# Kernel tuning notes

Measured on AMD Instinct MI355X. Metric: run time of the kernel, lower is better.

## Reference

```python
import jax, jax.numpy as jnp
import numpy as np

B, Q, K, H = 4, 128, 1024, 256
QS, KS, DV = 256, 256, 256


def setup_inputs() -> dict:
    key = jax.random.key(0)
    k1, k2, k3, k4, k5, k6, k7 = jax.random.split(key, 7)
    return {
        "queries": jax.random.normal(k1, (B, Q, QS), dtype=jnp.float32),
        "keys": jax.random.normal(k2, (B, K, KS), dtype=jnp.float32),
        "values": jax.random.normal(k3, (B, K, DV), dtype=jnp.float32),
        "valid_lens": jax.random.randint(k4, (B,), 1, K, dtype=jnp.int64),
        "Wq": jax.random.normal(k5, (QS, H), dtype=jnp.float32) / np.sqrt(QS),
        "Wk": jax.random.normal(k6, (KS, H), dtype=jnp.float32) / np.sqrt(KS),
        "Wv": jax.random.normal(k7, (H,), dtype=jnp.float32) / np.sqrt(H),
    }


def reference(queries, keys, values, valid_lens, Wq, Wk, Wv):
    # Projections: [B,Q,H] and [B,K,H]
    q = jnp.einsum("bqe,eh->bqh", queries, Wq)
    k = jnp.einsum("bke,eh->bkh", keys, Wk)
    # Broadcast add + tanh: [B,Q,K,H] intermediate (the kernel-headroom op)
    feats = jnp.tanh(q[:, :, None, :] + k[:, None, :, :])
    # hidden -> 1 reduction: scores [B,Q,K]
    scores = jnp.einsum("bqkh,h->bqk", feats, Wv)
    # masked softmax: positions >= valid_len set to -1e6 (as in sequence_mask)
    mask = jnp.arange(scores.shape[-1])[None, None, :] < valid_lens[:, None, None]
    scores = jnp.where(mask, scores, jnp.float32(-1e6))
    attn = jax.nn.softmax(scores, axis=-1)
    # dropout is identity in eval mode
    return jnp.einsum("bqk,bkv->bqv", attn, values)
```

## Files before the change

### kernel.cpp

```cpp
#include <hip/hip_runtime.h>

#define NB 4
#define NQ 128
#define NK 1024
#define NH 256
#define NE 256
#define NV 256

#define TSCALE 2.8853900817779268f
#define LOG2E  1.4426950408889634f

static __device__ __forceinline__ float fexp2(float x){ return __builtin_amdgcn_exp2f(x); }
static __device__ __forceinline__ float frcp (float x){ return __builtin_amdgcn_rcpf(x); }
static __device__ __forceinline__ float expT(float x){ return fexp2(x * TSCALE); }

__global__ __launch_bounds__(256) void proj_kernel(
    const float* __restrict__ qin, const float* __restrict__ kin,
    const float* __restrict__ Wq, const float* __restrict__ Wk,
    const float* __restrict__ Wv,
    float4* __restrict__ qEa, float4* __restrict__ kEt) {
    const int tid = threadIdx.x;
    const int bi  = blockIdx.x;
    __shared__ float tr[NH][9];
    if (bi < NB * 32) {
        const int row0 = bi * 4;
        const float* r0 = qin + row0 * NE;
        float a0 = 0.f, a1 = 0.f, a2 = 0.f, a3 = 0.f;
#pragma unroll 2
        for (int e = 0; e < NE; e += 4) {
            float4 q0 = *(const float4*)(r0 + e);
            float4 q1 = *(const float4*)(r0 + NE + e);
            float4 q2 = *(const float4*)(r0 + 2 * NE + e);
            float4 q3 = *(const float4*)(r0 + 3 * NE + e);
#pragma unroll
            for (int j = 0; j < 4; ++j) {
                float w = Wq[(e + j) * NH + tid];
                a0 = fmaf(((const float*)&q0)[j], w, a0);
                a1 = fmaf(((const float*)&q1)[j], w, a1);
                a2 = fmaf(((const float*)&q2)[j], w, a2);
                a3 = fmaf(((const float*)&q3)[j], w, a3);
            }
        }
        qEa[bi * NH + tid] = make_float4(expT(a0), expT(a1),
                                         expT(a2), expT(a3));
    } else {
        const int kb = bi - NB * 32;
        const int b  = kb >> 7;
        const int k0 = (kb & 127) * 8;
        const int c   = k0 >> 6;
        const int kl0 = k0 & 63;
        const float* kr = kin + (b * NK + k0) * NE;
        float acc[8] = {0.f,0.f,0.f,0.f,0.f,0.f,0.f,0.f};
#pragma unroll 2
        for (int e = 0; e < NE; e += 4) {
            float4 kvv[8];
#pragma unroll
            for (int i = 0; i < 8; ++i) kvv[i] = *(const float4*)(kr + i * NE + e);
#pragma unroll
            for (int j = 0; j < 4; ++j) {
                float w = Wk[(e + j) * NH + tid];
#pragma unroll
                for (int i = 0; i < 8; ++i)
                    acc[i] = fmaf(((const float*)&kvv[i])[j], w, acc[i]);
            }
        }
#pragma unroll
        for (int i = 0; i < 8; ++i) tr[tid][i] = expT(acc[i]);
        __syncthreads();
#pragma unroll
        for (int p = 0; p < 2; ++p) {
            int idx2 = p * 256 + tid;
            int hg = idx2 >> 3;
            int kk = idx2 & 7;
            float4 v = make_float4(tr[hg*4+0][kk], tr[hg*4+1][kk],
                                   tr[hg*4+2][kk], tr[hg*4+3][kk]);
            kEt[((b * 16 + c) * 64 + hg) * 64 + kl0 + kk] = v;
        }
    }
}

__global__ __launch_bounds__(256) void attn_kernel(
    const float4* __restrict__ qEa,
    const float4* __restrict__ kEt, const float* __restrict__ V,
    const int* __restrict__ vlen, const float4* __restrict__ Wv4,
    float* __restrict__ part_m, float* __restrict__ part_s,
    float* __restrict__ part_pv) {
    const int tid = threadIdx.x, lane = tid & 63, wvid = tid >> 6;
    const int n0 = (vlen[0] + 63) >> 6, n1 = (vlen[1] + 63) >> 6;
    const int n2 = (vlen[2] + 63) >> 6, n3 = (vlen[3] + 63) >> 6;
    const int G  = n0 + n1 + n2 + n3;
    const int bi = blockIdx.x;
    const int xcd = bi & 7;
    const int jj  = bi >> 3;
    const int qq  = jj & 31;
    const int gs  = ((jj >> 5) << 3) + xcd;
    if (gs >= G) return;
    int b, chunk;
    if      (gs < n0)           { b = 0; chunk = gs; }
    else if (gs < n0 + n1)      { b = 1; chunk = gs - n0; }
    else if (gs < n0 + n1 + n2) { b = 2; chunk = gs - n0 - n1; }
    else                        { b = 3; chunk = gs - n0 - n1 - n2; }
    const int vl    = vlen[b];
    const int k0    = chunk * 64;
    const int k     = k0 + lane;
    const int pidx  = (b * 32 + qq) * 16 + chunk;
    float* pm  = part_m + pidx * 4;
    float* ps  = part_s + pidx * 4;
    float* ppv = part_pv + pidx * (4 * NV);

    __shared__ float red17[4][64 * 17];
    __shared__ float pwT[64][4];
    __shared__ float4 qL[NH];

    qL[tid] = qEa[(b * 32 + qq) * NH + tid];
    __syncthreads();

    const float4* kp = kEt + ((b * 16 + chunk) * 64 + wvid * 16) * 64 + lane;
    float acc0 = 0.f, acc1 = 0.f, acc2 = 0.f, acc3 = 0.f;
#pragma unroll
    for (int i = 0; i < 16; ++i) {
        float4 kv4 = kp[i * 64];
        const int h4 = wvid * 16 + i;
        float4 wv4 = Wv4[h4];
#pragma unroll
        for (int j = 0; j < 4; ++j) {
            float kv  = (j==0)?kv4.x:(j==1)?kv4.y:(j==2)?kv4.z:kv4.w;
            float wvj = (j==0)?wv4.x:(j==1)?wv4.y:(j==2)?wv4.z:wv4.w;
            float4 qa = qL[h4 * 4 + j];
            float t0 = fmaf(qa.x, kv, 1.0f);
            float t1 = fmaf(qa.y, kv, 1.0f);
            float t2 = fmaf(qa.z, kv, 1.0f);
            float t3 = fmaf(qa.w, kv, 1.0f);
            float ab = t0 * t1, cd = t2 * t3;
            float rw = wvj * frcp(ab * cd);
            float rab = rw * cd, rcd = rw * ab;
            acc0 = fmaf(rab, t1, acc0);
            acc1 = fmaf(rab, t0, acc1);
            acc2 = fmaf(rcd, t3, acc2);
            acc3 = fmaf(rcd, t2, acc3);
        }
    }
    {
        float* hp = &red17[wvid][lane * 17];
        hp[0] = acc0; hp[1] = acc1; hp[2] = acc2; hp[3] = acc3;
    }
    __syncthreads();
    {
        const int row = wvid;
        float s = red17[0][lane * 17 + row] + red17[1][lane * 17 + row]
                + red17[2][lane * 17 + row] + red17[3][lane * 17 + row];
        s = (k < vl) ? (-2.0f * s) : -1e30f;
        float m = s;
#pragma unroll
        for (int d = 32; d >= 1; d >>= 1) m = fmaxf(m, __shfl_xor(m, d, 64));
        float p = fexp2((s - m) * LOG2E);
        float u = p;
#pragma unroll
        for (int d = 32; d >= 1; d >>= 1) u += __shfl_xor(u, d, 64);
        if (lane == 0) { pm[row] = m; ps[row] = u; }
        pwT[lane][row] = p;
    }
    __syncthreads();
    {
        const float* Vb = V + (b * NK + k0) * NV;
        const int v4 = lane * 4;
        float4 o0 = {0,0,0,0}, o1 = {0,0,0,0}, o2 = {0,0,0,0}, o3 = {0,0,0,0};
#pragma unroll 4
        for (int kk = 0; kk < 16; ++kk) {
            const int kkk = wvid * 16 + kk;
            float4 pv = *(const float4*)&pwT[kkk][0];
            float4 vv = *(const float4*)&Vb[kkk * NV + v4];
            o0.x = fmaf(pv.x, vv.x, o0.x); o0.y = fmaf(pv.x, vv.y, o0.y);
            o0.z = fmaf(pv.x, vv.z, o0.z); o0.w = fmaf(pv.x, vv.w, o0.w);
            o1.x = fmaf(pv.y, vv.x, o1.x); o1.y = fmaf(pv.y, vv.y, o1.y);
            o1.z = fmaf(pv.y, vv.z, o1.z); o1.w = fmaf(pv.y, vv.w, o1.w);
            o2.x = fmaf(pv.z, vv.x, o2.x); o2.y = fmaf(pv.z, vv.y, o2.y);
            o2.z = fmaf(pv.z, vv.z, o2.z); o2.w = fmaf(pv.z, vv.w, o2.w);
            o3.x = fmaf(pv.w, vv.x, o3.x); o3.y = fmaf(pv.w, vv.y, o3.y);
            o3.z = fmaf(pv.w, vv.z, o3.z); o3.w = fmaf(pv.w, vv.w, o3.w);
        }
        float* pd = &red17[wvid][lane * 17];
        *(float4*)(pd + 0)  = o0;
        *(float4*)(pd + 4)  = o1;
        *(float4*)(pd + 8)  = o2;
        *(float4*)(pd + 12) = o3;
    }
    __syncthreads();
    {
        const int row = tid >> 6, vg = tid & 63;
        float4 r = {0,0,0,0};
#pragma unroll
        for (int ww = 0; ww < 4; ++ww) {
            float4 t = *(const float4*)&red17[ww][vg * 17 + row * 4];
            r.x += t.x; r.y += t.y; r.z += t.z; r.w += t.w;
        }
        *(float4*)&ppv[row * NV + vg * 4] = r;
    }
}

__global__ __launch_bounds__(256) void combine_kernel(
    const float* __restrict__ part_m, const float* __restrict__ part_s,
    const float* __restrict__ part_pv, const int* __restrict__ vlen,
    float* __restrict__ out) {
    const int tid = threadIdx.x;
    const int idx = blockIdx.x;
    const int bi  = idx >> 2;
    const int i   = idx & 3;
    const int b   = bi >> 5;
    const int nb  = (vlen[b] + 63) >> 6;
    const int base = bi * 16;
    float M = -1e30f;
    for (int q = 0; q < nb; ++q)
        M = fmaxf(M, part_m[(base + q) * 4 + i]);
    float S = 0.f, o = 0.f;
    for (int q = 0; q < nb; ++q) {
        float wq = fexp2((part_m[(base + q) * 4 + i] - M) * LOG2E);
        S = fmaf(part_s[(base + q) * 4 + i], wq, S);
        o = fmaf(part_pv[((base + q) * 4 + i) * NV + tid], wq, o);
    }
    out[(bi * 4 + i) * NV + tid] = o * frcp(S);
}

extern "C" void kernel_launch(void* const* d_in, const int* in_sizes, int n_in,
                              void* d_out, int out_size, void* d_ws, size_t ws_size,
                              hipStream_t stream) {
    const float* queries = (const float*)d_in[0];
    const float* keys    = (const float*)d_in[1];
    const float* values  = (const float*)d_in[2];
    const int*   vlens   = (const int*)  d_in[3];
    const float* Wq      = (const float*)d_in[4];
    const float* Wk      = (const float*)d_in[5];
    const float* Wv      = (const float*)d_in[6];
    float* out = (float*)d_out;

    float4* qEa    = (float4*)d_ws;
    float4* kEt    = qEa + NB * 32 * NH;
    float*  part_m = (float*)(kEt + NB * 64 * NK);
    float*  part_s = part_m + 8192;
    float*  part_pv = part_s + 8192;

    proj_kernel   <<<dim3(640), dim3(256), 0, stream>>>(queries, keys, Wq, Wk, Wv,
                                                        qEa, kEt);
    attn_kernel   <<<dim3(2048), dim3(256), 0, stream>>>(qEa, kEt, values,
                                                         vlens, (const float4*)Wv,
                                                         part_m, part_s, part_pv);
    combine_kernel<<<dim3(512), dim3(256), 0, stream>>>(part_m, part_s, part_pv,
                                                        vlens, out);
}
```

Baseline: 113.3 us.

## Drop softmax max tracking using bounded scores, shrink key projection tile

```diff
diff --git a/kernel.cpp b/kernel.cpp
--- a/kernel.cpp
+++ b/kernel.cpp
@@ -7,8 +7,8 @@
 #define NE 256
 #define NV 256
 
-#define TSCALE 2.8853900817779268f
-#define LOG2E  1.4426950408889634f
+#define TSCALE     2.8853900817779268f
+#define NEG2LOG2E -2.8853900817779268f
 
 static __device__ __forceinline__ float fexp2(float x){ return __builtin_amdgcn_exp2f(x); }
 static __device__ __forceinline__ float frcp (float x){ return __builtin_amdgcn_rcpf(x); }
@@ -17,11 +17,10 @@
 __global__ __launch_bounds__(256) void proj_kernel(
     const float* __restrict__ qin, const float* __restrict__ kin,
     const float* __restrict__ Wq, const float* __restrict__ Wk,
-    const float* __restrict__ Wv,
     float4* __restrict__ qEa, float4* __restrict__ kEt) {
     const int tid = threadIdx.x;
     const int bi  = blockIdx.x;
-    __shared__ float tr[NH][9];
+    __shared__ float tr[NH][5];
     if (bi < NB * 32) {
         const int row0 = bi * 4;
         const float* r0 = qin + row0 * NE;
@@ -45,33 +44,31 @@
                                          expT(a2), expT(a3));
     } else {
         const int kb = bi - NB * 32;
-        const int b  = kb >> 7;
-        const int k0 = (kb & 127) * 8;
+        const int b  = kb >> 8;
+        const int k0 = (kb & 255) * 4;
         const int c   = k0 >> 6;
         const int kl0 = k0 & 63;
         const float* kr = kin + (b * NK + k0) * NE;
-        float acc[8] = {0.f,0.f,0.f,0.f,0.f,0.f,0.f,0.f};
+        float acc[4] = {0.f,0.f,0.f,0.f};
 #pragma unroll 2
         for (int e = 0; e < NE; e += 4) {
-            float4 kvv[8];
-#pragma unroll
-            for (int i = 0; i < 8; ++i) kvv[i] = *(const float4*)(kr + i * NE + e);
+            float4 kvv[4];
+#pragma unroll
+            for (int i = 0; i < 4; ++i) kvv[i] = *(const float4*)(kr + i * NE + e);
 #pragma unroll
             for (int j = 0; j < 4; ++j) {
                 float w = Wk[(e + j) * NH + tid];
 #pragma unroll
-                for (int i = 0; i < 8; ++i)
+                for (int i = 0; i < 4; ++i)
                     acc[i] = fmaf(((const float*)&kvv[i])[j], w, acc[i]);
             }
         }
 #pragma unroll
-        for (int i = 0; i < 8; ++i) tr[tid][i] = expT(acc[i]);
+        for (int i = 0; i < 4; ++i) tr[tid][i] = expT(acc[i]);
         __syncthreads();
-#pragma unroll
-        for (int p = 0; p < 2; ++p) {
-            int idx2 = p * 256 + tid;
-            int hg = idx2 >> 3;
-            int kk = idx2 & 7;
+        {
+            const int hg = tid >> 2;
+            const int kk = tid & 3;
             float4 v = make_float4(tr[hg*4+0][kk], tr[hg*4+1][kk],
                                    tr[hg*4+2][kk], tr[hg*4+3][kk]);
             kEt[((b * 16 + c) * 64 + hg) * 64 + kl0 + kk] = v;
@@ -83,8 +80,7 @@
     const float4* __restrict__ qEa,
     const float4* __restrict__ kEt, const float* __restrict__ V,
     const int* __restrict__ vlen, const float4* __restrict__ Wv4,
-    float* __restrict__ part_m, float* __restrict__ part_s,
-    float* __restrict__ part_pv) {
+    float* __restrict__ part_s, float* __restrict__ part_pv) {
     const int tid = threadIdx.x, lane = tid & 63, wvid = tid >> 6;
     const int n0 = (vlen[0] + 63) >> 6, n1 = (vlen[1] + 63) >> 6;
     const int n2 = (vlen[2] + 63) >> 6, n3 = (vlen[3] + 63) >> 6;
@@ -104,18 +100,14 @@
     const int k0    = chunk * 64;
     const int k     = k0 + lane;
     const int pidx  = (b * 32 + qq) * 16 + chunk;
-    float* pm  = part_m + pidx * 4;
     float* ps  = part_s + pidx * 4;
     float* ppv = part_pv + pidx * (4 * NV);
 
     __shared__ float red17[4][64 * 17];
     __shared__ float pwT[64][4];
-    __shared__ float4 qL[NH];
-
-    qL[tid] = qEa[(b * 32 + qq) * NH + tid];
-    __syncthreads();
 
     const float4* kp = kEt + ((b * 16 + chunk) * 64 + wvid * 16) * 64 + lane;
+    const float4* qp = qEa + (b * 32 + qq) * NH;
     float acc0 = 0.f, acc1 = 0.f, acc2 = 0.f, acc3 = 0.f;
 #pragma unroll
     for (int i = 0; i < 16; ++i) {
@@ -126,7 +118,7 @@
         for (int j = 0; j < 4; ++j) {
             float kv  = (j==0)?kv4.x:(j==1)?kv4.y:(j==2)?kv4.z:kv4.w;
             float wvj = (j==0)?wv4.x:(j==1)?wv4.y:(j==2)?wv4.z:wv4.w;
-            float4 qa = qL[h4 * 4 + j];
+            float4 qa = qp[h4 * 4 + j];
             float t0 = fmaf(qa.x, kv, 1.0f);
             float t1 = fmaf(qa.y, kv, 1.0f);
             float t2 = fmaf(qa.z, kv, 1.0f);
@@ -149,15 +141,13 @@
         const int row = wvid;
         float s = red17[0][lane * 17 + row] + red17[1][lane * 17 + row]
                 + red17[2][lane * 17 + row] + red17[3][lane * 17 + row];
-        s = (k < vl) ? (-2.0f * s) : -1e30f;
-        float m = s;
-#pragma unroll
-        for (int d = 32; d >= 1; d >>= 1) m = fmaxf(m, __shfl_xor(m, d, 64));
-        float p = fexp2((s - m) * LOG2E);
+        float x = s * NEG2LOG2E;
+        x = (k < vl) ? x : -1e38f;
+        float p = fexp2(x);
         float u = p;
 #pragma unroll
         for (int d = 32; d >= 1; d >>= 1) u += __shfl_xor(u, d, 64);
-        if (lane == 0) { pm[row] = m; ps[row] = u; }
+        if (lane == 0) ps[row] = u;
         pwT[lane][row] = p;
     }
     __syncthreads();
@@ -199,9 +189,8 @@
 }
 
 __global__ __launch_bounds__(256) void combine_kernel(
-    const float* __restrict__ part_m, const float* __restrict__ part_s,
-    const float* __restrict__ part_pv, const int* __restrict__ vlen,
-    float* __restrict__ out) {
+    const float* __restrict__ part_s, const float* __restrict__ part_pv,
+    const int* __restrict__ vlen, float* __restrict__ out) {
     const int tid = threadIdx.x;
     const int idx = blockIdx.x;
     const int bi  = idx >> 2;
@@ -209,14 +198,10 @@
     const int b   = bi >> 5;
     const int nb  = (vlen[b] + 63) >> 6;
     const int base = bi * 16;
-    float M = -1e30f;
-    for (int q = 0; q < nb; ++q)
-        M = fmaxf(M, part_m[(base + q) * 4 + i]);
     float S = 0.f, o = 0.f;
     for (int q = 0; q < nb; ++q) {
-        float wq = fexp2((part_m[(base + q) * 4 + i] - M) * LOG2E);
-        S = fmaf(part_s[(base + q) * 4 + i], wq, S);
-        o = fmaf(part_pv[((base + q) * 4 + i) * NV + tid], wq, o);
+        S += part_s[(base + q) * 4 + i];
+        o += part_pv[((base + q) * 4 + i) * NV + tid];
     }
     out[(bi * 4 + i) * NV + tid] = o * frcp(S);
 }
@@ -235,15 +220,14 @@
 
     float4* qEa    = (float4*)d_ws;
     float4* kEt    = qEa + NB * 32 * NH;
-    float*  part_m = (float*)(kEt + NB * 64 * NK);
-    float*  part_s = part_m + 8192;
+    float*  part_s = (float*)(kEt + NB * 64 * NK);
     float*  part_pv = part_s + 8192;
 
-    proj_kernel   <<<dim3(640), dim3(256), 0, stream>>>(queries, keys, Wq, Wk, Wv,
-                                                        qEa, kEt);
+    proj_kernel   <<<dim3(1152), dim3(256), 0, stream>>>(queries, keys, Wq, Wk,
+                                                         qEa, kEt);
     attn_kernel   <<<dim3(2048), dim3(256), 0, stream>>>(qEa, kEt, values,
                                                          vlens, (const float4*)Wv,
-                                                         part_m, part_s, part_pv);
-    combine_kernel<<<dim3(512), dim3(256), 0, stream>>>(part_m, part_s, part_pv,
+                                                         part_s, part_pv);
+    combine_kernel<<<dim3(512), dim3(256), 0, stream>>>(part_s, part_pv,
                                                         vlens, out);
 }
```

Result: no change. 112.5 us (median of 2 runs) (-0.7%).
